# Optimization experiments

Measured on AMD Instinct MI355X. Metric: run time of the kernel, lower is better.

## Reference

```python
import jax, jax.numpy as jnp
import numpy as np

NUM_NODES = 200000
NUM_EDGES = 600000
NUM_GRAPHS = 10000
BN_EPS = 1e-5


def setup_inputs() -> dict:
    key = jax.random.key(0)
    ks = jax.random.split(key, 10)
    x = jax.random.normal(ks[0], (NUM_NODES, 78), dtype=jnp.float32)
    edge_index = jax.random.randint(ks[1], (2, NUM_EDGES), 0, NUM_NODES, dtype=jnp.int64 if jax.config.jax_enable_x64 else jnp.int32)
    batch = jnp.sort(jax.random.randint(ks[2], (NUM_NODES,), 0, NUM_GRAPHS))
    def glorot(k, shape):
        fan_in, fan_out = shape[-2], shape[-1]
        s = jnp.sqrt(2.0 / (fan_in + fan_out))
        return jax.random.normal(k, shape, dtype=jnp.float32) * s
    return {
        "x": x,
        "edge_index": edge_index,
        "batch": batch,
        "W1_0": glorot(ks[3], (78, 128)),
        "b1_0": jnp.zeros((128,), jnp.float32),
        "W2_0": glorot(ks[4], (128, 128)),
        "b2_0": jnp.zeros((128,), jnp.float32),
        "g_0": jnp.ones((128,), jnp.float32),
        "be_0": jnp.zeros((128,), jnp.float32),
        "W1s": glorot(ks[5], (4, 128, 128)),
        "b1s": jnp.zeros((4, 128), jnp.float32),
        "W2s": glorot(ks[6], (4, 128, 128)),
        "b2s": jnp.zeros((4, 128), jnp.float32),
        "gs": jnp.ones((4, 128), jnp.float32),
        "bes": jnp.zeros((4, 128), jnp.float32),
        "fcW": glorot(ks[7], (128, 64)),
        "fcb": jnp.zeros((64,), jnp.float32),
    }


def _batchnorm(h, gamma, beta):
    # BatchNorm1d with batch statistics (training-mode normalization)
    mean = h.mean(axis=0)
    var = h.var(axis=0)  # biased, as torch uses for normalization
    return gamma * (h - mean) * jax.lax.rsqrt(var + BN_EPS) + beta


def _gin_block(h, src, dst, W1, b1, W2, b2, gamma, beta):
    # GINConv (eps=0): MLP(x + sum of neighbor messages), then ReLU + BN
    agg = jax.ops.segment_sum(h[src], dst, num_segments=NUM_NODES)  # [N, d]
    z = h + agg
    z = jax.nn.relu(z @ W1 + b1) @ W2 + b2
    z = jax.nn.relu(z)
    return _batchnorm(z, gamma, beta)


def reference(x, edge_index, batch, W1_0, b1_0, W2_0, b2_0, g_0, be_0,
              W1s, b1s, W2s, b2s, gs, bes, fcW, fcb):
    src, dst = edge_index[0], edge_index[1]
    h = _gin_block(x, src, dst, W1_0, b1_0, W2_0, b2_0, g_0, be_0)  # [N, 128]

    def body(h, params):
        W1, b1, W2, b2, g, be = params
        return _gin_block(h, src, dst, W1, b1, W2, b2, g, be), None

    h, _ = jax.lax.scan(body, h, (W1s, b1s, W2s, b2s, gs, bes))

    pooled = jax.ops.segment_sum(h, batch, num_segments=NUM_GRAPHS)  # [G, 128]
    out = jax.nn.relu(pooled @ fcW + fcb)  # [G, 64]; dropout is identity at eval
    return out
```

## Files before the change

### kernel.cpp

```cpp
#include <hip/hip_runtime.h>
#include <hip/hip_bf16.h>

#define NN 200000
#define NE 600000
#define NG 10000
#define NCH 98
#define NTILE 3125

typedef __attribute__((ext_vector_type(8))) short bfrag;
typedef __attribute__((ext_vector_type(4))) float f32x4;
typedef unsigned short u16;

static __device__ __forceinline__ u16 f2b(float x) {
  __hip_bfloat16 b = __float2bfloat16(x);
  return __builtin_bit_cast(u16, b);
}
static __device__ __forceinline__ float b2f(u16 u) {
  __hip_bfloat16 b = __builtin_bit_cast(__hip_bfloat16, u);
  return __bfloat162float(b);
}
static __device__ __forceinline__ void split(float v, u16& hi, u16& lo) {
  hi = f2b(v);
  lo = f2b(v - b2f(hi));
}

__global__ void prep_kernel(const float* __restrict__ W1_0, const float* __restrict__ W2_0,
                            const float* __restrict__ W1s, const float* __restrict__ W2s,
                            u16* __restrict__ wf) {
  int i = blockIdx.x * 256 + threadIdx.x;
  if (i >= 312 * 64) return;
  int t = i >> 6, lane = i & 63;
  const float* W;
  int KS, ct, kk, Krows, base, half;
  if (t < 24) {
    W = W1_0; KS = 3; ct = t / 3; kk = t - ct * 3; Krows = 78; base = 0; half = 12288;
  } else if (t < 56) {
    int u = t - 24;
    W = W2_0; KS = 4; ct = u >> 2; kk = u & 3; Krows = 128; base = 24576; half = 16384;
  } else {
    int u = t - 56;
    int j = u >> 6, r = u & 63;
    KS = 4; Krows = 128; half = 16384;
    if (r < 32) {
      W = W1s + j * 16384; ct = r >> 2; kk = r & 3; base = 57344 + j * 65536;
    } else {
      W = W2s + j * 16384; r -= 32; ct = r >> 2; kk = r & 3; base = 57344 + j * 65536 + 32768;
    }
  }
  int col = ct * 16 + (lane & 15);
  int idx = ((ct * KS + kk) * 64 + lane) * 8;
  for (int jj = 0; jj < 8; jj++) {
    int k = kk * 32 + 8 * (lane >> 4) + jj;
    float v = (k < Krows) ? W[k * 128 + col] : 0.f;
    u16 hi, lo;
    split(v, hi, lo);
    wf[base + idx + jj] = hi;
    wf[base + half + idx + jj] = lo;
  }
}

__global__ void hist_kernel(const int* __restrict__ dst, int* __restrict__ deg) {
  int e = blockIdx.x * 256 + threadIdx.x;
  if (e < NE) atomicAdd(&deg[dst[e]], 1);
}

__global__ void scan1_kernel(const int* __restrict__ deg, int* __restrict__ csum) {
  __shared__ int s[256];
  int base = blockIdx.x * 2048 + threadIdx.x * 8;
  int t = 0;
#pragma unroll
  for (int j = 0; j < 8; j++) {
    int idx = base + j;
    if (idx < NN) t += deg[idx];
  }
  s[threadIdx.x] = t;
  __syncthreads();
  for (int o = 128; o > 0; o >>= 1) {
    if (threadIdx.x < o) s[threadIdx.x] += s[threadIdx.x + o];
    __syncthreads();
  }
  if (threadIdx.x == 0) csum[blockIdx.x] = s[0];
}

__global__ void scan2_kernel(int* __restrict__ csum, int* __restrict__ rowptr) {
  int acc = 0;
  for (int i = 0; i < NCH; i++) {
    int v = csum[i];
    csum[i] = acc;
    acc += v;
  }
  rowptr[NN] = acc;
}

__global__ void scan3_kernel(const int* deg, const int* __restrict__ csum,
                             int* __restrict__ rowptr, int* cursor) {
  __shared__ int s[256];
  int tid = threadIdx.x;
  int base = blockIdx.x * 2048 + tid * 8;
  int loc[8];
  int t = 0;
#pragma unroll
  for (int j = 0; j < 8; j++) {
    int idx = base + j;
    int d = (idx < NN) ? deg[idx] : 0;
    loc[j] = t;
    t += d;
  }
  s[tid] = t;
  __syncthreads();
  for (int o = 1; o < 256; o <<= 1) {
    int u = (tid >= o) ? s[tid - o] : 0;
    __syncthreads();
    s[tid] += u;
    __syncthreads();
  }
  int off = csum[blockIdx.x] + s[tid] - t;
#pragma unroll
  for (int j = 0; j < 8; j++) {
    int idx = base + j;
    if (idx < NN) {
      int r = off + loc[j];
      rowptr[idx] = r;
      cursor[idx] = r;
    }
  }
}

__global__ void scatter_kernel(const int* __restrict__ src, const int* __restrict__ dst,
                               int* __restrict__ cursor, int* __restrict__ csr_src) {
  int e = blockIdx.x * 256 + threadIdx.x;
  if (e < NE) {
    int p = atomicAdd(&cursor[dst[e]], 1);
    csr_src[p] = src[e];
  }
}

template <bool FIRST>
__global__ __launch_bounds__(512, 4) void fused_kernel(
    const float* __restrict__ xin, const u16* __restrict__ hin,
    const float* __restrict__ ss,
    const int* __restrict__ rowptr, const int* __restrict__ csr_src,
    const u16* __restrict__ w1hi, const u16* __restrict__ w1lo,
    const u16* __restrict__ w2hi, const u16* __restrict__ w2lo,
    const float* __restrict__ b1, const float* __restrict__ b2,
    u16* __restrict__ hout, float* __restrict__ stats) {
  constexpr int KS1 = FIRST ? 3 : 4;
  constexpr int XH = 0, XL = 8704;
  __shared__ u16 lds[17408];
  const int tid = threadIdx.x;
  const int w = tid >> 6, l = tid & 63;
  const int l15 = l & 15, lg = l >> 4;
  const float bb1 = b1[w * 16 + l15];
  const float bb2 = b2[w * 16 + l15];
  float s_acc = 0.f, q_acc = 0.f;

  float sc8[8], sh8[8];
  if (!FIRST) {
    int k8 = l15 * 8;
#pragma unroll
    for (int j = 0; j < 8; j++) {
      sc8[j] = ss[k8 + j];
      sh8[j] = ss[128 + k8 + j];
    }
  }

  for (int tile = blockIdx.x; tile < NTILE; tile += gridDim.x) {
    const int rows0 = tile * 64;

    if (FIRST) {
      const float2* x2 = reinterpret_cast<const float2*>(xin);
      for (int j = 0; j < 8; j++) {
        int row = w * 8 + j;
        int node = rows0 + row;
        int beg = rowptr[node], end = rowptr[node + 1];
        int f0 = l * 2;
        if (f0 < 78) {
          size_t fv = (size_t)(f0 >> 1);
          float2 acc = x2[(size_t)node * 39 + fv];
          for (int i = beg; i < end; i += 4) {
            int last = end - 1;
            int i1 = min(i + 1, last), i2 = min(i + 2, last), i3 = min(i + 3, last);
            int s0 = csr_src[i], s1 = csr_src[i1], s2 = csr_src[i2], s3 = csr_src[i3];
            float2 v0 = x2[(size_t)s0 * 39 + fv];
            float2 v1 = x2[(size_t)s1 * 39 + fv];
            float2 v2 = x2[(size_t)s2 * 39 + fv];
            float2 v3 = x2[(size_t)s3 * 39 + fv];
            int rem = end - i;
            float m1 = rem > 1 ? 1.f : 0.f, m2 = rem > 2 ? 1.f : 0.f, m3 = rem > 3 ? 1.f : 0.f;
            acc.x += v0.x + m1 * v1.x + m2 * v2.x + m3 * v3.x;
            acc.y += v0.y + m1 * v1.y + m2 * v2.y + m3 * v3.y;
          }
          ushort2 oh, ol;
          split(acc.x, oh.x, ol.x);
          split(acc.y, oh.y, ol.y);
          *reinterpret_cast<ushort2*>(&lds[XH + row * 136 + f0]) = oh;
          *reinterpret_cast<ushort2*>(&lds[XL + row * 136 + f0]) = ol;
        } else if (f0 < 96) {
          ushort2 z = {0, 0};
          *reinterpret_cast<ushort2*>(&lds[XH + row * 136 + f0]) = z;
          *reinterpret_cast<ushort2*>(&lds[XL + row * 136 + f0]) = z;
        }
      }
    } else {
      const bfrag* hp = reinterpret_cast<const bfrag*>(hin);
      const int k8v = l15;
      for (int p = 0; p < 2; p++) {
        int row = w * 8 + p * 4 + lg;
        int node = rows0 + row;
        int beg = rowptr[node], end = rowptr[node + 1];
        float a[8];
        bfrag vs = hp[(size_t)node * 16 + k8v];
#pragma unroll
        for (int j = 0; j < 8; j++) a[j] = b2f((u16)vs[j]);
        for (int i = beg; i < end; i += 4) {
          int last = end - 1;
          int i1 = min(i + 1, last), i2 = min(i + 2, last), i3 = min(i + 3, last);
          int s0 = csr_src[i], s1 = csr_src[i1], s2 = csr_src[i2], s3 = csr_src[i3];
          bfrag v0 = hp[(size_t)s0 * 16 + k8v];
          bfrag v1 = hp[(size_t)s1 * 16 + k8v];
          bfrag v2 = hp[(size_t)s2 * 16 + k8v];
          bfrag v3 = hp[(size_t)s3 * 16 + k8v];
          int rem = end - i;
          float m1 = rem > 1 ? 1.f : 0.f, m2 = rem > 2 ? 1.f : 0.f, m3 = rem > 3 ? 1.f : 0.f;
#pragma unroll
          for (int j = 0; j < 8; j++)
            a[j] += (b2f((u16)v0[j]) + m1 * b2f((u16)v1[j])) +
                    (m2 * b2f((u16)v2[j]) + m3 * b2f((u16)v3[j]));
        }
        float cnt = (float)(end - beg + 1);
        bfrag oh, ol;
#pragma unroll
        for (int j = 0; j < 8; j++) {
          float t = a[j] * sc8[j] + cnt * sh8[j];
          u16 hi, lo;
          split(t, hi, lo);
          oh[j] = (short)hi;
          ol[j] = (short)lo;
        }
        *reinterpret_cast<bfrag*>(&lds[XH + row * 136 + l15 * 8]) = oh;
        *reinterpret_cast<bfrag*>(&lds[XL + row * 136 + l15 * 8]) = ol;
      }
    }
    bfrag w1h[KS1], w1l[KS1];
#pragma unroll
    for (int kk = 0; kk < KS1; kk++) {
      int fi = ((w * KS1 + kk) * 64 + l) * 8;
      w1h[kk] = *reinterpret_cast<const bfrag*>(&w1hi[fi]);
      w1l[kk] = *reinterpret_cast<const bfrag*>(&w1lo[fi]);
    }
    __syncthreads();

    f32x4 t1[4];
#pragma unroll
    for (int rt = 0; rt < 4; rt++) {
      f32x4 acc = {bb1, bb1, bb1, bb1};
      const int arow = (rt * 16 + l15) * 136 + 8 * lg;
#pragma unroll
      for (int kk = 0; kk < KS1; kk++) {
        bfrag ah = *reinterpret_cast<const bfrag*>(&lds[XH + arow + kk * 32]);
        bfrag al = *reinterpret_cast<const bfrag*>(&lds[XL + arow + kk * 32]);
        acc = __builtin_amdgcn_mfma_f32_16x16x32_bf16(al, w1h[kk], acc, 0, 0, 0);
        acc = __builtin_amdgcn_mfma_f32_16x16x32_bf16(ah, w1l[kk], acc, 0, 0, 0);
        acc = __builtin_amdgcn_mfma_f32_16x16x32_bf16(ah, w1h[kk], acc, 0, 0, 0);
      }
      t1[rt] = acc;
    }
    __syncthreads();

#pragma unroll
    for (int rt = 0; rt < 4; rt++) {
#pragma unroll
      for (int r = 0; r < 4; r++) {
        float v = fmaxf(t1[rt][r], 0.f);
        u16 hi, lo;
        split(v, hi, lo);
        int off = (rt * 16 + 4 * lg + r) * 136 + w * 16 + l15;
        lds[XH + off] = hi;
        lds[XL + off] = lo;
      }
    }
    bfrag w2h[4], w2l[4];
#pragma unroll
    for (int kk = 0; kk < 4; kk++) {
      int fi = ((w * 4 + kk) * 64 + l) * 8;
      w2h[kk] = *reinterpret_cast<const bfrag*>(&w2hi[fi]);
      w2l[kk] = *reinterpret_cast<const bfrag*>(&w2lo[fi]);
    }
    __syncthreads();

    u16 o16[16];
#pragma unroll
    for (int rt = 0; rt < 4; rt++) {
      f32x4 acc = {bb2, bb2, bb2, bb2};
      const int arow = (rt * 16 + l15) * 136 + 8 * lg;
#pragma unroll
      for (int kk = 0; kk < 4; kk++) {
        bfrag th = *reinterpret_cast<const bfrag*>(&lds[XH + arow + kk * 32]);
        bfrag tl = *reinterpret_cast<const bfrag*>(&lds[XL + arow + kk * 32]);
        acc = __builtin_amdgcn_mfma_f32_16x16x32_bf16(tl, w2h[kk], acc, 0, 0, 0);
        acc = __builtin_amdgcn_mfma_f32_16x16x32_bf16(th, w2l[kk], acc, 0, 0, 0);
        acc = __builtin_amdgcn_mfma_f32_16x16x32_bf16(th, w2h[kk], acc, 0, 0, 0);
      }
#pragma unroll
      for (int r = 0; r < 4; r++) {
        float v = fmaxf(acc[r], 0.f);
        s_acc += v;
        q_acc += v * v;
        o16[rt * 4 + r] = f2b(v);
      }
    }
    __syncthreads();

#pragma unroll
    for (int rt = 0; rt < 4; rt++) {
#pragma unroll
      for (int r = 0; r < 4; r++) {
        lds[XH + (rt * 16 + 4 * lg + r) * 136 + w * 16 + l15] = o16[rt * 4 + r];
      }
    }
    __syncthreads();

#pragma unroll
    for (int p = 0; p < 2; p++) {
      int row = p * 32 + (tid >> 4);
      int c8 = tid & 15;
      bfrag vv = *reinterpret_cast<const bfrag*>(&lds[XH + row * 136 + c8 * 8]);
      *reinterpret_cast<bfrag*>(&hout[(size_t)(rows0 + row) * 128 + c8 * 8]) = vv;
    }
    __syncthreads();
  }
  s_acc += __shfl_xor(s_acc, 16);
  s_acc += __shfl_xor(s_acc, 32);
  q_acc += __shfl_xor(q_acc, 16);
  q_acc += __shfl_xor(q_acc, 32);
  if (lg == 0) {
    atomicAdd(&stats[w * 16 + l15], s_acc);
    atomicAdd(&stats[128 + w * 16 + l15], q_acc);
  }
}

__global__ void bn_kernel(const float* __restrict__ stats, const float* __restrict__ gamma,
                          const float* __restrict__ beta, float* __restrict__ ss) {
  int c = threadIdx.x;
  float mean = stats[c] * (1.f / NN);
  float var = stats[128 + c] * (1.f / NN) - mean * mean;
  var = fmaxf(var, 0.f);
  float sc = gamma[c] * rsqrtf(var + 1e-5f);
  ss[c] = sc;
  ss[128 + c] = beta[c] - mean * sc;
}

__global__ void pool_kernel(const u16* __restrict__ h, const float* __restrict__ ss,
                            const int* __restrict__ batch, float* __restrict__ pooled) {
  int c = threadIdx.x;
  int n0 = blockIdx.x * 128;
  int n1 = min(n0 + 128, NN);
  float sc = ss[c], sh = ss[128 + c];
  float acc = 0.f;
  float cnt = 0.f;
  int gprev = batch[n0];
  for (int n = n0; n < n1; n++) {
    int g = batch[n];
    if (g != gprev) {
      atomicAdd(&pooled[gprev * 128 + c], sc * acc + cnt * sh);
      acc = 0.f;
      cnt = 0.f;
      gprev = g;
    }
    acc += b2f(h[(size_t)n * 128 + c]);
    cnt += 1.f;
  }
  atomicAdd(&pooled[gprev * 128 + c], sc * acc + cnt * sh);
}

__global__ void fc_kernel(const float* __restrict__ pooled, const float* __restrict__ fcW,
                          const float* __restrict__ fcb, float* __restrict__ out) {
  int i = blockIdx.x * 256 + threadIdx.x;
  if (i >= NG * 64) return;
  int g = i >> 6, o = i & 63;
  float acc = fcb[o];
#pragma unroll 8
  for (int k = 0; k < 128; k++) acc += pooled[g * 128 + k] * fcW[k * 64 + o];
  out[i] = fmaxf(acc, 0.f);
}

extern "C" void kernel_launch(void* const* d_in, const int* in_sizes, int n_in,
                              void* d_out, int out_size, void* d_ws, size_t ws_size,
                              hipStream_t stream) {
  const float* x = (const float*)d_in[0];
  const int* ei = (const int*)d_in[1];
  const int* src = ei;
  const int* dst = ei + NE;
  const int* batch = (const int*)d_in[2];
  const float* W1_0 = (const float*)d_in[3];
  const float* b1_0 = (const float*)d_in[4];
  const float* W2_0 = (const float*)d_in[5];
  const float* b2_0 = (const float*)d_in[6];
  const float* g_0 = (const float*)d_in[7];
  const float* be_0 = (const float*)d_in[8];
  const float* W1s = (const float*)d_in[9];
  const float* b1s = (const float*)d_in[10];
  const float* W2s = (const float*)d_in[11];
  const float* b2s = (const float*)d_in[12];
  const float* gs = (const float*)d_in[13];
  const float* bes = (const float*)d_in[14];
  const float* fcW = (const float*)d_in[15];
  const float* fcb = (const float*)d_in[16];

  char* ws = (char*)d_ws;
  u16* buf0 = (u16*)(ws + 0);
  u16* buf1 = (u16*)(ws + 51200000);
  float* POOLED = (float*)(ws + 102400000);
  float* STATS = (float*)(ws + 107520000);
  float* SS = (float*)(ws + 107521024);
  u16* WF = (u16*)(ws + 107522048);
  int* ROWPTR = (int*)(ws + 108161024);
  int* CURSOR = (int*)(ws + 108961040);
  int* CSRC = (int*)(ws + 109761040);
  int* CSUM = (int*)(ws + 112161040);

  prep_kernel<<<78, 256, 0, stream>>>(W1_0, W2_0, W1s, W2s, WF);

  hipMemsetAsync(CURSOR, 0, NN * 4, stream);
  hist_kernel<<<(NE + 255) / 256, 256, 0, stream>>>(dst, CURSOR);
  scan1_kernel<<<NCH, 256, 0, stream>>>(CURSOR, CSUM);
  scan2_kernel<<<1, 1, 0, stream>>>(CSUM, ROWPTR);
  scan3_kernel<<<NCH, 256, 0, stream>>>(CURSOR, CSUM, ROWPTR, CURSOR);
  scatter_kernel<<<(NE + 255) / 256, 256, 0, stream>>>(src, dst, CURSOR, CSRC);

  u16* buf[2] = {buf0, buf1};
  hipMemsetAsync(STATS, 0, 1024, stream);
  fused_kernel<true><<<512, 512, 0, stream>>>(x, nullptr, nullptr, ROWPTR, CSRC,
                                              WF, WF + 12288, WF + 24576, WF + 40960,
                                              b1_0, b2_0, buf0, STATS);
  bn_kernel<<<1, 128, 0, stream>>>(STATS, g_0, be_0, SS);

  for (int L = 1; L < 5; L++) {
    int j = L - 1;
    const u16* hin = buf[(L + 1) & 1];
    u16* hb = buf[L & 1];
    hipMemsetAsync(STATS, 0, 1024, stream);
    const u16* wl = WF + 57344 + j * 65536;
    fused_kernel<false><<<512, 512, 0, stream>>>(nullptr, hin, SS, ROWPTR, CSRC,
                                                 wl, wl + 16384, wl + 32768, wl + 49152,
                                                 b1s + j * 128, b2s + j * 128, hb, STATS);
    bn_kernel<<<1, 128, 0, stream>>>(STATS, gs + j * 128, bes + j * 128, SS);
  }

  hipMemsetAsync(POOLED, 0, (size_t)NG * 128 * 4, stream);
  pool_kernel<<<(NN + 127) / 128, 128, 0, stream>>>(buf[0], SS, batch, POOLED);
  fc_kernel<<<(NG * 64 + 255) / 256, 256, 0, stream>>>(POOLED, fcW, fcb, (float*)d_out);
}
```

Baseline: 668.9 us.

## Software-pipeline neighbor gather of next tile behind current tile's MLP

```diff
diff --git a/kernel.cpp b/kernel.cpp
--- a/kernel.cpp
+++ b/kernel.cpp
@@ -145,8 +145,8 @@
     const float* __restrict__ b1, const float* __restrict__ b2,
     u16* __restrict__ hout, float* __restrict__ stats) {
   constexpr int KS1 = FIRST ? 3 : 4;
-  constexpr int XH = 0, XL = 8704;
-  __shared__ u16 lds[17408];
+  constexpr int AH = 0, AL = 8704, TH = 17408, TL = 26112;
+  __shared__ u16 lds[34816];
   const int tid = threadIdx.x;
   const int w = tid >> 6, l = tid & 63;
   const int l15 = l & 15, lg = l >> 4;
@@ -154,21 +154,10 @@
   const float bb2 = b2[w * 16 + l15];
   float s_acc = 0.f, q_acc = 0.f;
 
-  float sc8[8], sh8[8];
-  if (!FIRST) {
-    int k8 = l15 * 8;
-#pragma unroll
-    for (int j = 0; j < 8; j++) {
-      sc8[j] = ss[k8 + j];
-      sh8[j] = ss[128 + k8 + j];
-    }
-  }
-
-  for (int tile = blockIdx.x; tile < NTILE; tile += gridDim.x) {
-    const int rows0 = tile * 64;
-
-    if (FIRST) {
-      const float2* x2 = reinterpret_cast<const float2*>(xin);
+  if (FIRST) {
+    const float2* x2 = reinterpret_cast<const float2*>(xin);
+    for (int tile = blockIdx.x; tile < NTILE; tile += gridDim.x) {
+      const int rows0 = tile * 64;
       for (int j = 0; j < 8; j++) {
         int row = w * 8 + j;
         int node = rows0 + row;
@@ -193,141 +182,309 @@
           ushort2 oh, ol;
           split(acc.x, oh.x, ol.x);
           split(acc.y, oh.y, ol.y);
-          *reinterpret_cast<ushort2*>(&lds[XH + row * 136 + f0]) = oh;
-          *reinterpret_cast<ushort2*>(&lds[XL + row * 136 + f0]) = ol;
+          *reinterpret_cast<ushort2*>(&lds[AH + row * 136 + f0]) = oh;
+          *reinterpret_cast<ushort2*>(&lds[AL + row * 136 + f0]) = ol;
         } else if (f0 < 96) {
           ushort2 z = {0, 0};
-          *reinterpret_cast<ushort2*>(&lds[XH + row * 136 + f0]) = z;
-          *reinterpret_cast<ushort2*>(&lds[XL + row * 136 + f0]) = z;
-        }
-      }
-    } else {
-      const bfrag* hp = reinterpret_cast<const bfrag*>(hin);
-      const int k8v = l15;
-      for (int p = 0; p < 2; p++) {
-        int row = w * 8 + p * 4 + lg;
-        int node = rows0 + row;
-        int beg = rowptr[node], end = rowptr[node + 1];
-        float a[8];
-        bfrag vs = hp[(size_t)node * 16 + k8v];
-#pragma unroll
-        for (int j = 0; j < 8; j++) a[j] = b2f((u16)vs[j]);
-        for (int i = beg; i < end; i += 4) {
-          int last = end - 1;
-          int i1 = min(i + 1, last), i2 = min(i + 2, last), i3 = min(i + 3, last);
-          int s0 = csr_src[i], s1 = csr_src[i1], s2 = csr_src[i2], s3 = csr_src[i3];
-          bfrag v0 = hp[(size_t)s0 * 16 + k8v];
-          bfrag v1 = hp[(size_t)s1 * 16 + k8v];
-          bfrag v2 = hp[(size_t)s2 * 16 + k8v];
-          bfrag v3 = hp[(size_t)s3 * 16 + k8v];
-          int rem = end - i;
-          float m1 = rem > 1 ? 1.f : 0.f, m2 = rem > 2 ? 1.f : 0.f, m3 = rem > 3 ? 1.f : 0.f;
-#pragma unroll
-          for (int j = 0; j < 8; j++)
-            a[j] += (b2f((u16)v0[j]) + m1 * b2f((u16)v1[j])) +
-                    (m2 * b2f((u16)v2[j]) + m3 * b2f((u16)v3[j]));
-        }
-        float cnt = (float)(end - beg + 1);
-        bfrag oh, ol;
-#pragma unroll
-        for (int j = 0; j < 8; j++) {
-          float t = a[j] * sc8[j] + cnt * sh8[j];
+          *reinterpret_cast<ushort2*>(&lds[AH + row * 136 + f0]) = z;
+          *reinterpret_cast<ushort2*>(&lds[AL + row * 136 + f0]) = z;
+        }
+      }
+      bfrag w1h[KS1], w1l[KS1];
+#pragma unroll
+      for (int kk = 0; kk < KS1; kk++) {
+        int fi = ((w * KS1 + kk) * 64 + l) * 8;
+        w1h[kk] = *reinterpret_cast<const bfrag*>(&w1hi[fi]);
+        w1l[kk] = *reinterpret_cast<const bfrag*>(&w1lo[fi]);
+      }
+      __syncthreads();
+#pragma unroll
+      for (int rt = 0; rt < 4; rt++) {
+        f32x4 acc = {bb1, bb1, bb1, bb1};
+        const int arow = (rt * 16 + l15) * 136 + 8 * lg;
+#pragma unroll
+        for (int kk = 0; kk < KS1; kk++) {
+          bfrag ah = *reinterpret_cast<const bfrag*>(&lds[AH + arow + kk * 32]);
+          bfrag al = *reinterpret_cast<const bfrag*>(&lds[AL + arow + kk * 32]);
+          acc = __builtin_amdgcn_mfma_f32_16x16x32_bf16(al, w1h[kk], acc, 0, 0, 0);
+          acc = __builtin_amdgcn_mfma_f32_16x16x32_bf16(ah, w1l[kk], acc, 0, 0, 0);
+          acc = __builtin_amdgcn_mfma_f32_16x16x32_bf16(ah, w1h[kk], acc, 0, 0, 0);
+        }
+#pragma unroll
+        for (int r = 0; r < 4; r++) {
+          float v = fmaxf(acc[r], 0.f);
           u16 hi, lo;
-          split(t, hi, lo);
-          oh[j] = (short)hi;
-          ol[j] = (short)lo;
-        }
-        *reinterpret_cast<bfrag*>(&lds[XH + row * 136 + l15 * 8]) = oh;
-        *reinterpret_cast<bfrag*>(&lds[XL + row * 136 + l15 * 8]) = ol;
-      }
+          split(v, hi, lo);
+          int off = (rt * 16 + 4 * lg + r) * 136 + w * 16 + l15;
+          lds[TH + off] = hi;
+          lds[TL + off] = lo;
+        }
+      }
+      bfrag w2h[4], w2l[4];
+#pragma unroll
+      for (int kk = 0; kk < 4; kk++) {
+        int fi = ((w * 4 + kk) * 64 + l) * 8;
+        w2h[kk] = *reinterpret_cast<const bfrag*>(&w2hi[fi]);
+        w2l[kk] = *reinterpret_cast<const bfrag*>(&w2lo[fi]);
+      }
+      __syncthreads();
+      u16 o16[16];
+#pragma unroll
+      for (int rt = 0; rt < 4; rt++) {
+        f32x4 acc = {bb2, bb2, bb2, bb2};
+        const int arow = (rt * 16 + l15) * 136 + 8 * lg;
+#pragma unroll
+        for (int kk = 0; kk < 4; kk++) {
+          bfrag th = *reinterpret_cast<const bfrag*>(&lds[TH + arow + kk * 32]);
+          bfrag tl = *reinterpret_cast<const bfrag*>(&lds[TL + arow + kk * 32]);
+          acc = __builtin_amdgcn_mfma_f32_16x16x32_bf16(tl, w2h[kk], acc, 0, 0, 0);
+          acc = __builtin_amdgcn_mfma_f32_16x16x32_bf16(th, w2l[kk], acc, 0, 0, 0);
+          acc = __builtin_amdgcn_mfma_f32_16x16x32_bf16(th, w2h[kk], acc, 0, 0, 0);
+        }
+#pragma unroll
+        for (int r = 0; r < 4; r++) {
+          float v = fmaxf(acc[r], 0.f);
+          s_acc += v;
+          q_acc += v * v;
+          o16[rt * 4 + r] = f2b(v);
+        }
+      }
+      __syncthreads();
+#pragma unroll
+      for (int rt = 0; rt < 4; rt++)
+#pragma unroll
+        for (int r = 0; r < 4; r++)
+          lds[TH + (rt * 16 + 4 * lg + r) * 136 + w * 16 + l15] = o16[rt * 4 + r];
+      __syncthreads();
+#pragma unroll
+      for (int p2 = 0; p2 < 2; p2++) {
+        int row = p2 * 32 + (tid >> 4);
+        int c8 = tid & 15;
+        bfrag vv = *reinterpret_cast<const bfrag*>(&lds[TH + row * 136 + c8 * 8]);
+        *reinterpret_cast<bfrag*>(&hout[(size_t)(rows0 + row) * 128 + c8 * 8]) = vv;
+      }
+      __syncthreads();
     }
-    bfrag w1h[KS1], w1l[KS1];
-#pragma unroll
-    for (int kk = 0; kk < KS1; kk++) {
-      int fi = ((w * KS1 + kk) * 64 + l) * 8;
-      w1h[kk] = *reinterpret_cast<const bfrag*>(&w1hi[fi]);
-      w1l[kk] = *reinterpret_cast<const bfrag*>(&w1lo[fi]);
+  } else {
+    const bfrag* hp = reinterpret_cast<const bfrag*>(hin);
+    const int k8v = l15;
+    const int k8 = l15 * 8;
+    float sc8[8], sh8[8];
+#pragma unroll
+    for (int j = 0; j < 8; j++) {
+      sc8[j] = ss[k8 + j];
+      sh8[j] = ss[128 + k8 + j];
+    }
+
+    int tile0 = blockIdx.x;
+#pragma unroll
+    for (int p = 0; p < 2; p++) {
+      int row = w * 8 + p * 4 + lg;
+      int node = tile0 * 64 + row;
+      int beg = rowptr[node], end = rowptr[node + 1];
+      float a[8];
+      bfrag vs = hp[(size_t)node * 16 + k8v];
+#pragma unroll
+      for (int j = 0; j < 8; j++) a[j] = b2f((u16)vs[j]);
+      for (int i = beg; i < end; i += 4) {
+        int last = end - 1;
+        int i1 = min(i + 1, last), i2 = min(i + 2, last), i3 = min(i + 3, last);
+        int s0 = csr_src[i], s1 = csr_src[i1], s2 = csr_src[i2], s3 = csr_src[i3];
+        bfrag v0 = hp[(size_t)s0 * 16 + k8v];
+        bfrag v1 = hp[(size_t)s1 * 16 + k8v];
+        bfrag v2 = hp[(size_t)s2 * 16 + k8v];
+        bfrag v3 = hp[(size_t)s3 * 16 + k8v];
+        int rem = end - i;
+        float m1 = rem > 1 ? 1.f : 0.f, m2 = rem > 2 ? 1.f : 0.f, m3 = rem > 3 ? 1.f : 0.f;
+#pragma unroll
+        for (int j = 0; j < 8; j++)
+          a[j] += (b2f((u16)v0[j]) + m1 * b2f((u16)v1[j])) +
+                  (m2 * b2f((u16)v2[j]) + m3 * b2f((u16)v3[j]));
+      }
+      float cnt = (float)(end - beg + 1);
+      bfrag oh, ol;
+#pragma unroll
+      for (int j = 0; j < 8; j++) {
+        float t = a[j] * sc8[j] + cnt * sh8[j];
+        u16 hi, lo;
+        split(t, hi, lo);
+        oh[j] = (short)hi;
+        ol[j] = (short)lo;
+      }
+      *reinterpret_cast<bfrag*>(&lds[AH + row * 136 + k8]) = oh;
+      *reinterpret_cast<bfrag*>(&lds[AL + row * 136 + k8]) = ol;
     }
     __syncthreads();
 
-    f32x4 t1[4];
-#pragma unroll
-    for (int rt = 0; rt < 4; rt++) {
-      f32x4 acc = {bb1, bb1, bb1, bb1};
-      const int arow = (rt * 16 + l15) * 136 + 8 * lg;
-#pragma unroll
-      for (int kk = 0; kk < KS1; kk++) {
-        bfrag ah = *reinterpret_cast<const bfrag*>(&lds[XH + arow + kk * 32]);
-        bfrag al = *reinterpret_cast<const bfrag*>(&lds[XL + arow + kk * 32]);
-        acc = __builtin_amdgcn_mfma_f32_16x16x32_bf16(al, w1h[kk], acc, 0, 0, 0);
-        acc = __builtin_amdgcn_mfma_f32_16x16x32_bf16(ah, w1l[kk], acc, 0, 0, 0);
-        acc = __builtin_amdgcn_mfma_f32_16x16x32_bf16(ah, w1h[kk], acc, 0, 0, 0);
-      }
-      t1[rt] = acc;
+    for (int tile = tile0; tile < NTILE; tile += gridDim.x) {
+      const int rows0 = tile * 64;
+      int tn = tile + gridDim.x;
+      bool np = tn < NTILE;
+      int tnc = np ? tn : tile;
+
+      int begN[2], endN[2];
+#pragma unroll
+      for (int p = 0; p < 2; p++) {
+        int nodeN = tnc * 64 + w * 8 + p * 4 + lg;
+        begN[p] = rowptr[nodeN];
+        endN[p] = rowptr[nodeN + 1];
+      }
+
+      bfrag w1h[4], w1l[4];
+#pragma unroll
+      for (int kk = 0; kk < 4; kk++) {
+        int fi = ((w * 4 + kk) * 64 + l) * 8;
+        w1h[kk] = *reinterpret_cast<const bfrag*>(&w1hi[fi]);
+        w1l[kk] = *reinterpret_cast<const bfrag*>(&w1lo[fi]);
+      }
+      f32x4 t1[4];
+#pragma unroll
+      for (int rt = 0; rt < 4; rt++) {
+        f32x4 acc = {bb1, bb1, bb1, bb1};
+        const int arow = (rt * 16 + l15) * 136 + 8 * lg;
+#pragma unroll
+        for (int kk = 0; kk < 4; kk++) {
+          bfrag ah = *reinterpret_cast<const bfrag*>(&lds[AH + arow + kk * 32]);
+          bfrag al = *reinterpret_cast<const bfrag*>(&lds[AL + arow + kk * 32]);
+          acc = __builtin_amdgcn_mfma_f32_16x16x32_bf16(al, w1h[kk], acc, 0, 0, 0);
+          acc = __builtin_amdgcn_mfma_f32_16x16x32_bf16(ah, w1l[kk], acc, 0, 0, 0);
+          acc = __builtin_amdgcn_mfma_f32_16x16x32_bf16(ah, w1h[kk], acc, 0, 0, 0);
+        }
+        t1[rt] = acc;
+      }
+      __syncthreads();
+
+      int s0[2], s1[2], s2[2], s3[2];
+      float m0[2], m1[2], m2[2], m3[2], cntN[2];
+#pragma unroll
+      for (int p = 0; p < 2; p++) {
+        int beg = begN[p], end = endN[p];
+        int deg = end - beg;
+        int last = end - 1;
+        int i0 = beg, i1 = min(beg + 1, last), i2 = min(beg + 2, last), i3 = min(beg + 3, last);
+        if (deg <= 0) { i0 = 0; i1 = 0; i2 = 0; i3 = 0; }
+        s0[p] = csr_src[i0];
+        s1[p] = csr_src[i1];
+        s2[p] = csr_src[i2];
+        s3[p] = csr_src[i3];
+        m0[p] = deg > 0 ? 1.f : 0.f;
+        m1[p] = deg > 1 ? 1.f : 0.f;
+        m2[p] = deg > 2 ? 1.f : 0.f;
+        m3[p] = deg > 3 ? 1.f : 0.f;
+        cntN[p] = (float)(deg + 1);
+      }
+
+#pragma unroll
+      for (int rt = 0; rt < 4; rt++) {
+#pragma unroll
+        for (int r = 0; r < 4; r++) {
+          float v = fmaxf(t1[rt][r], 0.f);
+          u16 hi, lo;
+          split(v, hi, lo);
+          int off = (rt * 16 + 4 * lg + r) * 136 + w * 16 + l15;
+          lds[TH + off] = hi;
+          lds[TL + off] = lo;
+        }
+      }
+      bfrag w2h[4], w2l[4];
+#pragma unroll
+      for (int kk = 0; kk < 4; kk++) {
+        int fi = ((w * 4 + kk) * 64 + l) * 8;
+        w2h[kk] = *reinterpret_cast<const bfrag*>(&w2hi[fi]);
+        w2l[kk] = *reinterpret_cast<const bfrag*>(&w2lo[fi]);
+      }
+      __syncthreads();
+
+      bfrag selfN[2], nb0[2], nb1[2], nb2[2], nb3[2];
+#pragma unroll
+      for (int p = 0; p < 2; p++) {
+        int nodeN = tnc * 64 + w * 8 + p * 4 + lg;
+        selfN[p] = hp[(size_t)nodeN * 16 + k8v];
+        nb0[p] = hp[(size_t)s0[p] * 16 + k8v];
+        nb1[p] = hp[(size_t)s1[p] * 16 + k8v];
+        nb2[p] = hp[(size_t)s2[p] * 16 + k8v];
+        nb3[p] = hp[(size_t)s3[p] * 16 + k8v];
+      }
+
+      u16 o16[16];
+#pragma unroll
+      for (int rt = 0; rt < 4; rt++) {
+        f32x4 acc = {bb2, bb2, bb2, bb2};
+        const int arow = (rt * 16 + l15) * 136 + 8 * lg;
+#pragma unroll
+        for (int kk = 0; kk < 4; kk++) {
+          bfrag th = *reinterpret_cast<const bfrag*>(&lds[TH + arow + kk * 32]);
+          bfrag tl = *reinterpret_cast<const bfrag*>(&lds[TL + arow + kk * 32]);
+          acc = __builtin_amdgcn_mfma_f32_16x16x32_bf16(tl, w2h[kk], acc, 0, 0, 0);
+          acc = __builtin_amdgcn_mfma_f32_16x16x32_bf16(th, w2l[kk], acc, 0, 0, 0);
+          acc = __builtin_amdgcn_mfma_f32_16x16x32_bf16(th, w2h[kk], acc, 0, 0, 0);
+        }
+#pragma unroll
+        for (int r = 0; r < 4; r++) {
+          float v = fmaxf(acc[r], 0.f);
+          s_acc += v;
+          q_acc += v * v;
+          o16[rt * 4 + r] = f2b(v);
+        }
+      }
+      __syncthreads();
+
+      if (np) {
+#pragma unroll
+        for (int p = 0; p < 2; p++) {
+          int row = w * 8 + p * 4 + lg;
+          float a[8];
+#pragma unroll
+          for (int j = 0; j < 8; j++) a[j] = b2f((u16)selfN[p][j]);
+#pragma unroll
+          for (int j = 0; j < 8; j++)
+            a[j] += (m0[p] * b2f((u16)nb0[p][j]) + m1[p] * b2f((u16)nb1[p][j])) +
+                    (m2[p] * b2f((u16)nb2[p][j]) + m3[p] * b2f((u16)nb3[p][j]));
+          int beg = begN[p], end = endN[p];
+          for (int i = beg + 4; i < end; i += 4) {
+            int last = end - 1;
+            int i1 = min(i + 1, last), i2 = min(i + 2, last), i3 = min(i + 3, last);
+            int t0 = csr_src[i], t1i = csr_src[i1], t2 = csr_src[i2], t3 = csr_src[i3];
+            bfrag v0 = hp[(size_t)t0 * 16 + k8v];
+            bfrag v1 = hp[(size_t)t1i * 16 + k8v];
+            bfrag v2 = hp[(size_t)t2 * 16 + k8v];
+            bfrag v3 = hp[(size_t)t3 * 16 + k8v];
+            int rem = end - i;
+            float n1 = rem > 1 ? 1.f : 0.f, n2 = rem > 2 ? 1.f : 0.f, n3 = rem > 3 ? 1.f : 0.f;
+#pragma unroll
+            for (int j = 0; j < 8; j++)
+              a[j] += (b2f((u16)v0[j]) + n1 * b2f((u16)v1[j])) +
+                      (n2 * b2f((u16)v2[j]) + n3 * b2f((u16)v3[j]));
+          }
+          bfrag oh, ol;
+#pragma unroll
+          for (int j = 0; j < 8; j++) {
+            float t = a[j] * sc8[j] + cntN[p] * sh8[j];
+            u16 hi, lo;
+            split(t, hi, lo);
+            oh[j] = (short)hi;
+            ol[j] = (short)lo;
+          }
+          *reinterpret_cast<bfrag*>(&lds[AH + row * 136 + k8]) = oh;
+          *reinterpret_cast<bfrag*>(&lds[AL + row * 136 + k8]) = ol;
+        }
+      }
+
+#pragma unroll
+      for (int rt = 0; rt < 4; rt++)
+#pragma unroll
+        for (int r = 0; r < 4; r++)
+          lds[TH + (rt * 16 + 4 * lg + r) * 136 + w * 16 + l15] = o16[rt * 4 + r];
+      __syncthreads();
+
+#pragma unroll
+      for (int p2 = 0; p2 < 2; p2++) {
+        int row = p2 * 32 + (tid >> 4);
+        int c8 = tid & 15;
+        bfrag vv = *reinterpret_cast<const bfrag*>(&lds[TH + row * 136 + c8 * 8]);
+        *reinterpret_cast<bfrag*>(&hout[(size_t)(rows0 + row) * 128 + c8 * 8]) = vv;
+      }
     }
-    __syncthreads();
-
-#pragma unroll
-    for (int rt = 0; rt < 4; rt++) {
-#pragma unroll
-      for (int r = 0; r < 4; r++) {
-        float v = fmaxf(t1[rt][r], 0.f);
-        u16 hi, lo;
-        split(v, hi, lo);
-        int off = (rt * 16 + 4 * lg + r) * 136 + w * 16 + l15;
-        lds[XH + off] = hi;
-        lds[XL + off] = lo;
-      }
-    }
-    bfrag w2h[4], w2l[4];
-#pragma unroll
-    for (int kk = 0; kk < 4; kk++) {
-      int fi = ((w * 4 + kk) * 64 + l) * 8;
-      w2h[kk] = *reinterpret_cast<const bfrag*>(&w2hi[fi]);
-      w2l[kk] = *reinterpret_cast<const bfrag*>(&w2lo[fi]);
-    }
-    __syncthreads();
-
-    u16 o16[16];
-#pragma unroll
-    for (int rt = 0; rt < 4; rt++) {
-      f32x4 acc = {bb2, bb2, bb2, bb2};
-      const int arow = (rt * 16 + l15) * 136 + 8 * lg;
-#pragma unroll
-      for (int kk = 0; kk < 4; kk++) {
-        bfrag th = *reinterpret_cast<const bfrag*>(&lds[XH + arow + kk * 32]);
-        bfrag tl = *reinterpret_cast<const bfrag*>(&lds[XL + arow + kk * 32]);
-        acc = __builtin_amdgcn_mfma_f32_16x16x32_bf16(tl, w2h[kk], acc, 0, 0, 0);
-        acc = __builtin_amdgcn_mfma_f32_16x16x32_bf16(th, w2l[kk], acc, 0, 0, 0);
-        acc = __builtin_amdgcn_mfma_f32_16x16x32_bf16(th, w2h[kk], acc, 0, 0, 0);
-      }
-#pragma unroll
-      for (int r = 0; r < 4; r++) {
-        float v = fmaxf(acc[r], 0.f);
-        s_acc += v;
-        q_acc += v * v;
-        o16[rt * 4 + r] = f2b(v);
-      }
-    }
-    __syncthreads();
-
-#pragma unroll
-    for (int rt = 0; rt < 4; rt++) {
-#pragma unroll
-      for (int r = 0; r < 4; r++) {
-        lds[XH + (rt * 16 + 4 * lg + r) * 136 + w * 16 + l15] = o16[rt * 4 + r];
-      }
-    }
-    __syncthreads();
-
-#pragma unroll
-    for (int p = 0; p < 2; p++) {
-      int row = p * 32 + (tid >> 4);
-      int c8 = tid & 15;
-      bfrag vv = *reinterpret_cast<const bfrag*>(&lds[XH + row * 136 + c8 * 8]);
-      *reinterpret_cast<bfrag*>(&hout[(size_t)(rows0 + row) * 128 + c8 * 8]) = vv;
-    }
-    __syncthreads();
   }
   s_acc += __shfl_xor(s_acc, 16);
   s_acc += __shfl_xor(s_acc, 32);
```

Result: slower. 740.2 us (+10.7%).
